# Kernel tuning notes

Measured on AMD Instinct MI355X. Metric: run time of the kernel, lower is better.

## Reference

```python
import jax, jax.numpy as jnp
import numpy as np

B, V, S = 128, 64, 40
D, H, VOC = 256, 256, 20000


def setup_inputs() -> dict:
    key = jax.random.key(0)
    ks = jax.random.split(key, 26)
    g = lambda k, shp: (jax.random.normal(k, shp, dtype=jnp.float32) * 0.02)
    inp = {}
    inp['input_seqs'] = jax.random.randint(ks[0], (B, V, S), 0, VOC + 1)
    inp['mask'] = jnp.zeros((B, V), jnp.float32)
    inp['length'] = jax.random.randint(ks[1], (B,), 1, V + 1)
    inp['seq_time_step'] = jax.random.uniform(ks[2], (B, V), dtype=jnp.float32)
    inp['codemask'] = jnp.zeros((B, V, S), jnp.float32)
    inp['label'] = jax.random.randint(ks[3], (B,), 0, 2)
    # embedding table; padding_idx=-1 in torch == row VOC zeroed
    inp['emb'] = g(ks[4], (VOC + 1, D)).at[VOC].set(0.0)
    # LSTM (single layer, batch_first): torch gate order i,f,g,o
    inp['W_ih'] = g(ks[5], (4 * H, D))
    inp['W_hh'] = g(ks[6], (4 * H, H))
    inp['b_ih'] = g(ks[7], (4 * H,))
    inp['b_hh'] = g(ks[8], (4 * H,))
    # attention projections
    inp['Whk'] = g(ks[9], (D, H))
    inp['bhk'] = g(ks[10], (D,))
    inp['W1'] = g(ks[11], (64, 2 * H))
    inp['b1'] = g(ks[12], (64,))
    inp['W2'] = g(ks[13], (2, 64))
    inp['b2'] = g(ks[14], (2,))
    # classifyer MLP: d -> 4d -> 2d -> 2
    inp['C1W'] = g(ks[15], (4 * D, D))
    inp['C1b'] = g(ks[16], (4 * D,))
    inp['C2W'] = g(ks[17], (2 * D, 4 * D))
    inp['C2b'] = g(ks[18], (2 * D,))
    inp['CoW'] = g(ks[19], (2, 2 * D))
    inp['Cob'] = g(ks[20], (2,))
    return inp


def _lstm(x, W_ih, W_hh, b_ih, b_hh):
    # x: [B,T,D] -> hs: [B,T,H]; torch gate order i,f,g,o
    Bsz = x.shape[0]
    Hd = W_hh.shape[1]
    xg = jnp.einsum('btd,gd->btg', x, W_ih) + b_ih + b_hh  # [B,T,4H]

    def step(carry, xg_t):
        h, c = carry
        gates = xg_t + h @ W_hh.T
        i, f, gg, o = jnp.split(gates, 4, axis=-1)
        i = jax.nn.sigmoid(i); f = jax.nn.sigmoid(f)
        gg = jnp.tanh(gg); o = jax.nn.sigmoid(o)
        c = f * c + i * gg
        h = o * jnp.tanh(c)
        return (h, c), h

    z = jnp.zeros((Bsz, Hd), x.dtype)
    _, hs = jax.lax.scan(step, (z, z), jnp.swapaxes(xg, 0, 1))
    return jnp.swapaxes(hs, 0, 1)


def _classify(h, C1W, C1b, C2W, C2b, CoW, Cob):
    h = jax.nn.relu(h @ C1W.T + C1b)
    h = jax.nn.relu(h @ C2W.T + C2b)
    return h @ CoW.T + Cob


def reference(input_seqs, mask, length, seq_time_step, codemask, label,
              emb, W_ih, W_hh, b_ih, b_hh, Whk, bhk, W1, b1, W2, b2,
              C1W, C1b, C2W, C2b, CoW, Cob):
    # before(): embedding gather -> relu -> sum over codes (eval mode, no dropout)
    v = jax.nn.relu(emb[input_seqs]).sum(-2)  # [B,V,D]
    h = _lstm(v, W_ih, W_hh, b_ih, b_hh)       # [B,V,H]

    # vectorized form of the per-timestep attention loop:
    # bar_v[:,0]=v[:,0]; for i>=1: mix of e_k=v[:,0] and w_hk(h[:,i-1])
    e_k = v[:, :1, :]                                   # [B,1,D]
    wh = h @ Whk.T + bhk                                # [B,V,D]
    wh_prev = wh[:, :-1, :]                             # [B,V-1,D] (h at i-1)
    e_b = jnp.broadcast_to(e_k, wh_prev.shape)
    cat = jnp.concatenate([e_b, wh_prev], axis=-1)      # [B,V-1,2D]
    attn = jax.nn.softmax(jnp.tanh(cat @ W1.T + b1) @ W2.T + b2, axis=-1)
    bar_rest = e_b * attn[..., 0:1] + wh_prev * attn[..., 1:2]
    bar_v = jnp.concatenate([v[:, :1, :], bar_rest], axis=1)  # [B,V,D]

    # GAN stand-in (external injected module): identity
    Dec_V, Gen_V = bar_v, bar_v
    gen_h = _lstm(Gen_V, W_ih, W_hh, b_ih, b_hh)

    og = _classify(h, C1W, C1b, C2W, C2b, CoW, Cob)        # [B,V,2]
    fake = _classify(gen_h, C1W, C1b, C2W, C2b, CoW, Cob)  # [B,V,2]
    final_og = og[:, -1, :]
    final_fake = fake[:, -1, :]
    return (final_og, final_fake, Dec_V, Gen_V, seq_time_step, label)
```

## Files before the change

### kernel.cpp

```cpp
#include <hip/hip_runtime.h>

#define DEV __device__ __forceinline__

typedef float f32x4 __attribute__((ext_vector_type(4)));
typedef short s16x8 __attribute__((ext_vector_type(8)));
typedef short s16x4 __attribute__((ext_vector_type(4)));

DEV unsigned short f2bf(float f){
  unsigned int u = __float_as_uint(f);
  u += 0x7fffu + ((u>>16)&1u);
  return (unsigned short)(u>>16);
}
DEV float bf2f(unsigned short h){ return __uint_as_float(((unsigned int)h)<<16); }

#if __has_builtin(__builtin_amdgcn_rcpf)
DEV float frcp_(float x){ return __builtin_amdgcn_rcpf(x); }
#else
DEV float frcp_(float x){ return 1.f/x; }
#endif
#if __has_builtin(__builtin_amdgcn_exp2f)
DEV float fexp2_(float x){ return __builtin_amdgcn_exp2f(x); }
#else
DEV float fexp2_(float x){ return exp2f(x); }
#endif

DEV float tanh_(float x){
  x = fminf(x, 30.f);
  float e = fexp2_(2.8853900817779268f*x);
  return (e-1.f)*frcp_(e+1.f);
}

DEV unsigned char f2e4m3(float x){
  unsigned int u = __float_as_uint(x);
  unsigned int s = (u>>24)&0x80u;
  unsigned int mag = u & 0x7fffffffu;
  if (mag > 0x43E00000u) mag = 0x43E00000u;
  mag += 0x000FFFFFu + ((mag>>20)&1u);
  int e = (int)(mag>>23) - 120;
  unsigned int m = (mag>>20)&7u;
  unsigned int r = (e<=0) ? 0u : (((unsigned)e<<3)|m);
  return (unsigned char)(s|r);
}

DEV f32x4 mfma_bf16(s16x8 a, s16x8 b, f32x4 c){
  return __builtin_amdgcn_mfma_f32_16x16x32_bf16(a,b,c,0,0,0);
}
DEV f32x4 mfma_fp8(long a, long b, f32x4 c){
  return __builtin_amdgcn_mfma_f32_16x16x32_fp8_fp8(a,b,c,0,0,0);
}

DEV void lds_barrier(){
  asm volatile("s_waitcnt lgkmcnt(0)\n\ts_barrier" ::: "memory");
}

DEV unsigned aload_rlx(unsigned* p){
  return __hip_atomic_load(p, __ATOMIC_RELAXED, __HIP_MEMORY_SCOPE_AGENT);
}
DEV void astore_rel(unsigned* p, unsigned v){
  __hip_atomic_store(p, v, __ATOMIC_RELEASE, __HIP_MEMORY_SCOPE_AGENT);
}
DEV void aadd_rel(unsigned* p, unsigned v){
  __hip_atomic_fetch_add(p, v, __ATOMIC_RELEASE, __HIP_MEMORY_SCOPE_AGENT);
}
DEV void acq_fence(){ __builtin_amdgcn_fence(__ATOMIC_ACQUIRE, "agent"); }
DEV void spin_rlx(unsigned* p, unsigned tgt){
  while (aload_rlx(p) < tgt) __builtin_amdgcn_s_sleep(8);
  asm volatile("" ::: "memory");
}
template<int FENCE>
DEV void block_wait_ge(unsigned* p, unsigned tgt){
  if (threadIdx.x == 0){
    spin_rlx(p, tgt);
    if (FENCE) acq_fence();
  }
  __syncthreads();
}
DEV s16x4 aload64(const unsigned short* p){
  unsigned long long v = __hip_atomic_load((unsigned long long*)(void*)p,
      __ATOMIC_RELAXED, __HIP_MEMORY_SCOPE_AGENT);
  union { unsigned long long u; s16x4 s; } c; c.u = v; return c.s;
}

#define Bx 128
#define Vx 64
#define Sx 40
#define Dx 256
#define Hx 256
#define NVOC 20001

#define OFF_OG   0
#define OFF_FAKE 256
#define OFF_DECV 512
#define OFF_GENV 2097664
#define OFF_STS  4194816
#define OFF_LBL  4203008

#define PW_IH  0
#define PW_HH  262144
#define PW_HK  524288
#define PW_1   589824
#define PC_1   622592
#define PC_2   884736
#define PC_O   1409024
#define P_TOT  1410048

#define HPB 264
#define WHP 272

#define FCT(t) ((t)*32)
#define FBV(t) (2048 + (t)*32)
#define FXG(t) (4096 + (t)*32)
#define FUC    6144
#define FTOT   8192

__global__ void k_cvt_emb(const float* __restrict__ emb, unsigned short* __restrict__ emb16){
  size_t i = (size_t)blockIdx.x*256 + threadIdx.x;
  emb16[i] = f2bf(emb[i]);
}

__global__ void k_pre(const int* __restrict__ seqs, const unsigned short* __restrict__ emb16,
                      unsigned short* __restrict__ v16,
                      float* __restrict__ decv, float* __restrict__ genv,
                      unsigned short* __restrict__ barv16,
                      const float* __restrict__ W_ih, const float* __restrict__ Whh,
                      const float* __restrict__ Whk, const float* __restrict__ W1,
                      const float* __restrict__ C1W, const float* __restrict__ C2W,
                      const float* __restrict__ CoW,
                      unsigned short* __restrict__ pool, unsigned char* __restrict__ whh8,
                      const float* __restrict__ sts, const int* __restrict__ label,
                      float* __restrict__ out, unsigned* __restrict__ flags){
  int bx = blockIdx.x, tid = threadIdx.x;
  if (bx < 8192){
    int bt = bx, d = tid;
    const int* sp = seqs + (size_t)bt*Sx;
    float acc = 0.f;
    #pragma unroll 8
    for (int s=0;s<Sx;s++) acc += fmaxf(bf2f(emb16[(size_t)sp[s]*Dx + d]), 0.f);
    size_t o = (size_t)bt*Dx + d;
    v16[o] = f2bf(acc);
    if ((bt & 63) == 0){ decv[o] = acc; genv[o] = acc; barv16[o] = f2bf(acc); }
    return;
  }
  if (bx < 14724){
    int i = (bx-8192)*256 + tid;
    if (i < P_TOT){
      float v;
      if      (i < PW_HH) v = W_ih[i - PW_IH];
      else if (i < PW_HK) v = Whh [i - PW_HH];
      else if (i < PW_1 ) v = Whk [i - PW_HK];
      else if (i < PC_1 ) v = W1  [i - PW_1 ];
      else if (i < PC_2 ) v = C1W [i - PC_1 ];
      else if (i < PC_O ) v = C2W [i - PC_2 ];
      else                v = CoW [i - PC_O ];
      pool[i] = f2bf(v);
    } else if (i < P_TOT + 262144){
      whh8[i - P_TOT] = f2e4m3(16.f*Whh[i - P_TOT]);
    }
    return;
  }
  for (int i=tid;i<FTOT;i+=256) flags[i] = (i==FBV(0)) ? 1u : 0u;
  for (int i=tid;i<Bx*Vx;i+=256) out[OFF_STS + i] = sts[i];
  if (tid < Bx) out[OFF_LBL + tid] = (float)label[tid];
}

template<int MODE_A, int MODE_C, int RELU>
__global__ void k_gemm(const unsigned short* __restrict__ A, const unsigned short* __restrict__ Bw,
                       const float* __restrict__ bias1, const float* __restrict__ bias2,
                       unsigned short* __restrict__ C, int K, int Ntot, float scale){
  int tid = threadIdx.x, w = tid>>6, l = tid&63, lm = l&15, q = l>>4;
  int m0 = blockIdx.x*64;
  int n0 = blockIdx.y*256 + w*64;
  f32x4 acc[4][4];
  #pragma unroll
  for (int nt=0;nt<4;nt++){
    int n = n0 + nt*16 + lm;
    float bz = bias1 ? bias1[n] : 0.f;
    if (bias2) bz += bias2[n];
    #pragma unroll
    for (int mt=0;mt<4;mt++) acc[mt][nt] = (f32x4){bz,bz,bz,bz};
  }
  const s16x8* Arow[4];
  #pragma unroll
  for (int mt=0;mt<4;mt++){
    int m = m0 + mt*16 + lm;
    size_t off = (MODE_A==0) ? (size_t)m*K : ((size_t)(m&127)*Vx + (m>>7))*(size_t)K;
    Arow[mt] = (const s16x8*)(A + off);
  }
  int kkn = K/32;
  for (int kk=0; kk<kkn; kk++){
    s16x8 bfr[4];
    #pragma unroll
    for (int nt=0;nt<4;nt++){
      int n = n0 + nt*16 + lm;
      bfr[nt] = *(const s16x8*)(Bw + (size_t)n*K + kk*32 + q*8);
    }
    #pragma unroll
    for (int mt=0;mt<4;mt++){
      s16x8 afr = Arow[mt][kk*4 + q];
      #pragma unroll
      for (int nt=0;nt<4;nt++)
        acc[mt][nt] = mfma_bf16(afr, bfr[nt], acc[mt][nt]);
    }
  }
  #pragma unroll
  for (int mt=0;mt<4;mt++){
    int mbase = m0 + mt*16 + q*4;
    #pragma unroll
    for (int nt=0;nt<4;nt++){
      int n = n0 + nt*16 + lm;
      if (MODE_C==0){
        #pragma unroll
        for (int r=0;r<4;r++){
          float val = scale*acc[mt][nt][r];
          if (RELU) val = fmaxf(val, 0.f);
          C[(size_t)(mbase+r)*Ntot + n] = f2bf(val);
        }
      } else {
        int tt = mbase>>7, bb = mbase&127;
        int gg = bb>>4;
        s16x4 sv;
        #pragma unroll
        for (int r=0;r<4;r++) sv[r] = (short)f2bf(scale*acc[mt][nt][r]);
        *(s16x4*)(C + (((size_t)tt*8 + gg)*1024 + n)*16 + (bb&15)) = sv;
      }
    }
  }
}

template<int IS1>
DEV void scan_body(unsigned char* hl, const unsigned char* __restrict__ W8,
                   const unsigned short* __restrict__ xg, unsigned short* __restrict__ hist,
                   int g, unsigned* __restrict__ flags){
  int tid = threadIdx.x;
  int w = tid>>6, l = tid&63, lm = l&15, q = l>>4;
  int j = w*16 + lm;
  for (int i=tid;i<2*16*HPB;i+=1024) hl[i] = 0;
  long Bf[4][8];
  #pragma unroll
  for (int qq=0;qq<4;qq++){
    int n = qq*256 + j;
    #pragma unroll
    for (int kk=0;kk<8;kk++)
      Bf[qq][kk] = *(const long*)(W8 + (size_t)n*256 + kk*32 + q*8);
  }
  float cst[4] = {0.f,0.f,0.f,0.f};
  const unsigned short* xgb = xg + (size_t)g*16384 + q*4;
  s16x4 xc[4], xn[4];
  if (!IS1) block_wait_ge<0>(&flags[FXG(0)], 1);
  #pragma unroll
  for (int qq=0;qq<4;qq++){
    const unsigned short* p = xgb + (qq*256+j)*16;
    xc[qq] = IS1 ? *(const s16x4*)p : aload64(p);
  }
  __syncthreads();
  const float K1 = 1.4426950408889634f/256.f;
  const unsigned char* hrd = hl + lm*HPB + q*8;
  #pragma unroll 1
  for (int t=0;t<Vx;t++){
    if (t < Vx-1){
      if (!IS1) block_wait_ge<0>(&flags[FXG(t+1)], 1);
      #pragma unroll
      for (int qq=0;qq<4;qq++){
        const unsigned short* p = xgb + (size_t)(t+1)*131072 + (qq*256+j)*16;
        xn[qq] = IS1 ? *(const s16x4*)p : aload64(p);
      }
    }
    const unsigned char* hb = hrd + (t&1)*(16*HPB);
    f32x4 a0, a1, a2, a3;
    #pragma unroll
    for (int r=0;r<4;r++){
      a0[r] = bf2f((unsigned short)xc[0][r]);
      a1[r] = bf2f((unsigned short)xc[1][r]);
      a2[r] = bf2f((unsigned short)xc[2][r]);
      a3[r] = bf2f((unsigned short)xc[3][r]);
    }
    #pragma unroll
    for (int kk=0;kk<8;kk++){
      long af = *(const long*)(hb + kk*32);
      a0 = mfma_fp8(af, Bf[0][kk], a0);
      a1 = mfma_fp8(af, Bf[1][kk], a1);
      a2 = mfma_fp8(af, Bf[2][kk], a2);
      a3 = mfma_fp8(af, Bf[3][kk], a3);
    }
    unsigned char* hn = hl + ((t+1)&1)*(16*HPB) + j;
    float hv16[4];
    #pragma unroll
    for (int r=0;r<4;r++){
      float iv = frcp_(1.f + fexp2_(-K1*a0[r]));
      float fv = frcp_(1.f + fexp2_(-K1*a1[r]));
      float eg = fexp2_(2.f*K1*a2[r]);
      float gv = (eg-1.f)*frcp_(eg+1.f);
      float ov = frcp_(1.f + fexp2_(-K1*a3[r]));
      float cv = fv*cst[r] + iv*gv;
      cst[r] = cv;
      float ec = fexp2_(2.8853900817779268f*fminf(cv,30.f));
      float hv = ov*(ec-1.f)*frcp_(ec+1.f);
      hv16[r] = 16.f*hv;
      if (IS1)
        hist[((size_t)t*Bx + g*16 + q*4 + r)*Hx + j] = f2bf(hv);
      else if (t==Vx-1)
        hist[((size_t)(g*16 + q*4 + r))*Hx + j] = f2bf(hv);
    }
#if __has_builtin(__builtin_amdgcn_cvt_pk_fp8_f32)
    int p01 = __builtin_amdgcn_cvt_pk_fp8_f32(hv16[0], hv16[1], 0, false);
    int p23 = __builtin_amdgcn_cvt_pk_fp8_f32(hv16[2], hv16[3], 0, false);
    hn[(q*4+0)*HPB] = (unsigned char)p01;
    hn[(q*4+1)*HPB] = (unsigned char)(p01>>8);
    hn[(q*4+2)*HPB] = (unsigned char)p23;
    hn[(q*4+3)*HPB] = (unsigned char)(p23>>8);
#else
    #pragma unroll
    for (int r=0;r<4;r++) hn[(q*4+r)*HPB] = f2e4m3(hv16[r]);
#endif
    #pragma unroll
    for (int qq=0;qq<4;qq++) xc[qq] = xn[qq];
    if (IS1){
      __syncthreads();
      if (tid == 0) aadd_rel(&flags[FCT(t)], 1);
    } else {
      lds_barrier();
    }
  }
}

DEV void worker_body(unsigned short* whs, int t,
    const unsigned short* __restrict__ hist1, const unsigned short* __restrict__ v16,
    const float* __restrict__ u, const unsigned short* __restrict__ pool,
    const float* __restrict__ bhk, const float* __restrict__ W2, const float* __restrict__ b2,
    const float* __restrict__ b_ih, const float* __restrict__ b_hh,
    float* __restrict__ decv, float* __restrict__ genv,
    unsigned short* __restrict__ barv16, unsigned short* __restrict__ xg2,
    unsigned* flags){
  int tid = threadIdx.x, w = tid>>6, l = tid&63, lm = l&15, q = l>>4;
  if (t < 63){
    block_wait_ge<1>(&flags[FCT(t)], 8);
    int r0 = (w&7)*16, n0 = (w>>3)*128;
    const s16x8* Arow = (const s16x8*)(hist1 + ((size_t)t*Bx + r0 + lm)*Hx);
    f32x4 acc[8];
    #pragma unroll
    for (int nt=0;nt<8;nt++){
      float bz = bhk[n0 + nt*16 + lm];
      acc[nt] = (f32x4){bz,bz,bz,bz};
    }
    #pragma unroll
    for (int kk=0;kk<8;kk++){
      s16x8 afr = Arow[kk*4 + q];
      #pragma unroll
      for (int nt=0;nt<8;nt++){
        int n = n0 + nt*16 + lm;
        s16x8 bfr = *(const s16x8*)(pool + PW_HK + (size_t)n*256 + kk*32 + q*8);
        acc[nt] = mfma_bf16(afr, bfr, acc[nt]);
      }
    }
    #pragma unroll
    for (int nt=0;nt<8;nt++){
      int n = n0 + nt*16 + lm, mb = r0 + q*4;
      #pragma unroll
      for (int r=0;r<4;r++) whs[(size_t)(mb+r)*WHP + n] = f2bf(acc[nt][r]);
    }
    if (tid == 0){ spin_rlx(&flags[FUC], 8); acq_fence(); }
    __syncthreads();
    if (w < 8){
      int m0l = w*16;
      f32x4 a2[4];
      #pragma unroll
      for (int nt=0;nt<4;nt++){
        int n = nt*16 + lm;
        #pragma unroll
        for (int r=0;r<4;r++) a2[nt][r] = u[(size_t)(m0l + q*4 + r)*64 + n];
      }
      #pragma unroll
      for (int kk=0;kk<8;kk++){
        s16x8 afr = *(const s16x8*)(whs + (size_t)(m0l+lm)*WHP + kk*32 + q*8);
        #pragma unroll
        for (int nt=0;nt<4;nt++){
          int n = nt*16 + lm;
          s16x8 bfr = *(const s16x8*)(pool + PW_1 + (size_t)n*512 + 256 + kk*32 + q*8);
          a2[nt] = mfma_bf16(afr, bfr, a2[nt]);
        }
      }
      float p0a[4] = {0,0,0,0}, p1a[4] = {0,0,0,0};
      #pragma unroll
      for (int nt=0;nt<4;nt++){
        int n = nt*16 + lm;
        float w2a = W2[n], w2b = W2[64+n];
        #pragma unroll
        for (int r=0;r<4;r++){
          float z = tanh_(a2[nt][r]);
          p0a[r] += z*w2a; p1a[r] += z*w2b;
        }
      }
      #pragma unroll
      for (int s=1;s<16;s<<=1){
        #pragma unroll
        for (int r=0;r<4;r++){ p0a[r] += __shfl_xor(p0a[r], s, 16); p1a[r] += __shfl_xor(p1a[r], s, 16); }
      }
      float bb0 = b2[0], bb1 = b2[1];
      int d0 = lm*16;
      #pragma unroll
      for (int r=0;r<4;r++){
        int b = m0l + q*4 + r;
        float g0 = p0a[r]+bb0, g1 = p1a[r]+bb1;
        float al0 = frcp_(1.f + fexp2_(1.4426950408889634f*(g1-g0)));
        float al1 = 1.f - al0;
        const unsigned short* ek  = v16 + (size_t)b*Vx*Dx + d0;
        const unsigned short* whp = whs + (size_t)b*WHP + d0;
        size_t ob = ((size_t)b*Vx + (t+1))*Dx + d0;
        #pragma unroll
        for (int c=0;c<2;c++){
          s16x8 e8 = *(const s16x8*)(ek + c*8);
          s16x8 w8 = *(const s16x8*)(whp + c*8);
          s16x8 o16;
          #pragma unroll
          for (int jj=0;jj<8;jj++){
            float o = al0*bf2f((unsigned short)e8[jj]) + al1*bf2f((unsigned short)w8[jj]);
            decv[ob + c*8 + jj] = o;
            genv[ob + c*8 + jj] = o;
            o16[jj] = (short)f2bf(o);
          }
          *(s16x8*)(barv16 + ob + c*8) = o16;
        }
      }
    }
    __syncthreads();
    if (tid == 0) astore_rel(&flags[FBV(t+1)], 1);
  }
  block_wait_ge<1>(&flags[FBV(t)], 1);
  int mh = (w&1)*64, nb = (w>>1)*128;
  const s16x8* Arow2[4];
  #pragma unroll
  for (int mt=0;mt<4;mt++)
    Arow2[mt] = (const s16x8*)(barv16 + ((size_t)(mh + mt*16 + lm)*Vx + t)*Dx);
  #pragma unroll 1
  for (int sc=0; sc<4; sc++){
    int n0 = nb + sc*32;
    f32x4 acc[4][2];
    #pragma unroll
    for (int nt=0;nt<2;nt++){
      int n = n0 + nt*16 + lm;
      float bz = b_ih[n] + b_hh[n];
      #pragma unroll
      for (int mt=0;mt<4;mt++) acc[mt][nt] = (f32x4){bz,bz,bz,bz};
    }
    #pragma unroll
    for (int kk=0;kk<8;kk++){
      s16x8 bfr[2];
      #pragma unroll
      for (int nt=0;nt<2;nt++){
        int n = n0 + nt*16 + lm;
        bfr[nt] = *(const s16x8*)(pool + PW_IH + (size_t)n*256 + kk*32 + q*8);
      }
      #pragma unroll
      for (int mt=0;mt<4;mt++){
        s16x8 afr = Arow2[mt][kk*4 + q];
        acc[mt][0] = mfma_bf16(afr, bfr[0], acc[mt][0]);
        acc[mt][1] = mfma_bf16(afr, bfr[1], acc[mt][1]);
      }
    }
    #pragma unroll
    for (int mt=0;mt<4;mt++){
      int m = mh + mt*16 + q*4;
      int gg = m>>4;
      #pragma unroll
      for (int nt=0;nt<2;nt++){
        int n = n0 + nt*16 + lm;
        s16x4 sv;
        #pragma unroll
        for (int r=0;r<4;r++) sv[r] = (short)f2bf(256.f*acc[mt][nt][r]);
        *(s16x4*)(xg2 + (((size_t)t*8 + gg)*1024 + n)*16 + (m&15)) = sv;
      }
    }
  }
  __syncthreads();
  if (tid == 0) astore_rel(&flags[FXG(t)], 1);
}

__global__ __launch_bounds__(1024) void k_mega(
    const unsigned char* __restrict__ W8,
    const unsigned short* __restrict__ xg1, unsigned short* __restrict__ xg2,
    unsigned short* __restrict__ hist1, unsigned short* __restrict__ h2,
    const unsigned short* __restrict__ v16, float* __restrict__ u,
    const unsigned short* __restrict__ pool,
    const float* __restrict__ bhk, const float* __restrict__ W2, const float* __restrict__ b2,
    const float* __restrict__ b1, const float* __restrict__ b_ih, const float* __restrict__ b_hh,
    float* __restrict__ decv, float* __restrict__ genv, unsigned short* __restrict__ barv16,
    unsigned* __restrict__ flags){
  __shared__ __align__(16) unsigned char smem[69632];
  int blk = blockIdx.x;
  if (blk < 8){
    scan_body<1>(smem, W8, xg1, hist1, blk, flags);
  } else if (blk < 16){
    scan_body<0>(smem, W8, xg2, h2, blk-8, flags);
  } else if (blk < 80){
    worker_body((unsigned short*)smem, blk-16, hist1, v16, u, pool, bhk, W2, b2,
                b_ih, b_hh, decv, genv, barv16, xg2, flags);
  } else {
    int t2 = (blk-80)*1024 + threadIdx.x;
    int b = t2>>6, n = t2&63;
    const s16x8* vr = (const s16x8*)(v16 + (size_t)b*Vx*Dx);
    const s16x8* wr = (const s16x8*)(pool + PW_1 + (size_t)n*512);
    float a = b1[n];
    for (int kk=0;kk<32;kk++){
      s16x8 x = vr[kk], ww = wr[kk];
      #pragma unroll
      for (int jj=0;jj<8;jj++) a += bf2f((unsigned short)x[jj])*bf2f((unsigned short)ww[jj]);
    }
    u[t2] = a;
    __syncthreads();
    if (threadIdx.x == 0) aadd_rel(&flags[FUC], 1);
  }
}

__global__ void k_out(const unsigned short* __restrict__ y2, const unsigned short* __restrict__ CoW16,
                      const float* __restrict__ Cob, float* __restrict__ out){
  int tid = blockIdx.x*256 + threadIdx.x;
  int m = tid>>1, n = tid&1;
  const s16x8* yr = (const s16x8*)(y2 + (size_t)m*512);
  const s16x8* wr = (const s16x8*)(CoW16 + (size_t)n*512);
  float a = Cob[n];
  for (int kk=0;kk<64;kk++){
    s16x8 yv = yr[kk], ww = wr[kk];
    #pragma unroll
    for (int jj=0;jj<8;jj++) a += bf2f((unsigned short)yv[jj])*bf2f((unsigned short)ww[jj]);
  }
  int base = (m < 128) ? (OFF_OG + m*2) : (OFF_FAKE + (m-128)*2);
  out[base + n] = a;
}

extern "C" void kernel_launch(void* const* d_in, const int* in_sizes, int n_in,
                              void* d_out, int out_size, void* d_ws, size_t ws_size,
                              hipStream_t stream) {
  const int*   seqs  = (const int*)d_in[0];
  const float* sts   = (const float*)d_in[3];
  const int*   label = (const int*)d_in[5];
  const float* emb   = (const float*)d_in[6];
  const float* W_ih  = (const float*)d_in[7];
  const float* W_hh  = (const float*)d_in[8];
  const float* b_ih  = (const float*)d_in[9];
  const float* b_hh  = (const float*)d_in[10];
  const float* Whk   = (const float*)d_in[11];
  const float* bhk   = (const float*)d_in[12];
  const float* W1    = (const float*)d_in[13];
  const float* b1    = (const float*)d_in[14];
  const float* W2    = (const float*)d_in[15];
  const float* b2    = (const float*)d_in[16];
  const float* C1b   = (const float*)d_in[18];
  const float* C2b   = (const float*)d_in[20];
  const float* Cob   = (const float*)d_in[22];
  float* out = (float*)d_out;

  char* ws = (char*)d_ws;
  unsigned short* v16    = (unsigned short*)(ws + 0);
  unsigned short* xg1    = (unsigned short*)(ws + (4<<20));
  unsigned short* hist1  = (unsigned short*)(ws + (20<<20));
  unsigned short* barv16 = (unsigned short*)(ws + (25<<20));
  unsigned short* xg2    = (unsigned short*)(ws + (29<<20));
  unsigned short* emb16  = xg2;
  float*          u      = (float*)(ws + (45<<20));
  unsigned char*  whh8   = (unsigned char*)(ws + (45<<20) + (64<<10));
  unsigned*       flags  = (unsigned*)(ws + (45<<20) + (384<<10));
  unsigned short* pool   = (unsigned short*)(ws + (46<<20));
  unsigned short* y1     = xg1;
  unsigned short* y2     = xg1 + 262144;

  unsigned short* h2 = hist1 + (size_t)Vx*Bx*Hx;
  unsigned short* X  = hist1 + (size_t)(Vx-1)*Bx*Hx;

  float* decv = out + OFF_DECV;
  float* genv = out + OFF_GENV;

  k_cvt_emb<<<dim3(NVOC), dim3(256), 0, stream>>>(emb, emb16);
  k_pre<<<dim3(14725), dim3(256), 0, stream>>>(seqs, emb16, v16, decv, genv, barv16,
      W_ih, W_hh, Whk, W1, (const float*)d_in[17], (const float*)d_in[19],
      (const float*)d_in[21], pool, whh8, sts, label, out, flags);
  k_gemm<1,1,0><<<dim3(128,4), dim3(256), 0, stream>>>(v16, pool+PW_IH, b_ih, b_hh, xg1, 256, 1024, 256.f);
  k_mega<<<dim3(88), dim3(1024), 0, stream>>>(whh8, xg1, xg2, hist1, h2, v16, u, pool,
      bhk, W2, b2, b1, b_ih, b_hh, decv, genv, barv16, flags);
  k_gemm<0,0,1><<<dim3(4,4), dim3(256), 0, stream>>>(X, pool+PC_1, C1b, nullptr, y1, 256, 1024, 1.f);
  k_gemm<0,0,1><<<dim3(4,2), dim3(256), 0, stream>>>(y1, pool+PC_2, C2b, nullptr, y2, 1024, 512, 1.f);
  k_out<<<dim3(2), dim3(256), 0, stream>>>(y2, pool+PC_O, Cob, out);
}
```

Baseline: 537.4 us.

## Replace release/acquire fences with relaxed agent-scope atomics for cross-block data

Every value passed between blocks (hidden-state history, u, bar_v, xg2) is now written and read with relaxed agent-scope atomic loads and stores. This lets the flag signals drop their release/acquire semantics and the acquire fence, removing cache writeback and invalidate costs on the serial scan critical path. History stores are packed into 32-bit words through a lane shuffle, and 128-bit loads are split into two 64-bit atomic loads. The risk is memory-ordering correctness, because relaxed flags give no formal happens-before guarantee.

```diff
diff --git a/kernel.cpp b/kernel.cpp
--- a/kernel.cpp
+++ b/kernel.cpp
@@ -56,29 +56,44 @@
 DEV unsigned aload_rlx(unsigned* p){
   return __hip_atomic_load(p, __ATOMIC_RELAXED, __HIP_MEMORY_SCOPE_AGENT);
 }
-DEV void astore_rel(unsigned* p, unsigned v){
-  __hip_atomic_store(p, v, __ATOMIC_RELEASE, __HIP_MEMORY_SCOPE_AGENT);
-}
-DEV void aadd_rel(unsigned* p, unsigned v){
-  __hip_atomic_fetch_add(p, v, __ATOMIC_RELEASE, __HIP_MEMORY_SCOPE_AGENT);
-}
-DEV void acq_fence(){ __builtin_amdgcn_fence(__ATOMIC_ACQUIRE, "agent"); }
+DEV void astore_rlx(unsigned* p, unsigned v){
+  __hip_atomic_store(p, v, __ATOMIC_RELAXED, __HIP_MEMORY_SCOPE_AGENT);
+}
+DEV void aadd_rlx(unsigned* p, unsigned v){
+  __hip_atomic_fetch_add(p, v, __ATOMIC_RELAXED, __HIP_MEMORY_SCOPE_AGENT);
+}
 DEV void spin_rlx(unsigned* p, unsigned tgt){
   while (aload_rlx(p) < tgt) __builtin_amdgcn_s_sleep(8);
   asm volatile("" ::: "memory");
 }
-template<int FENCE>
 DEV void block_wait_ge(unsigned* p, unsigned tgt){
-  if (threadIdx.x == 0){
-    spin_rlx(p, tgt);
-    if (FENCE) acq_fence();
-  }
+  if (threadIdx.x == 0) spin_rlx(p, tgt);
   __syncthreads();
 }
-DEV s16x4 aload64(const unsigned short* p){
+DEV void wt_store32(unsigned short* p, unsigned v){
+  __hip_atomic_store((unsigned*)(void*)p, v, __ATOMIC_RELAXED, __HIP_MEMORY_SCOPE_AGENT);
+}
+DEV void wt_store32f(float* p, float v){
+  __hip_atomic_store(p, v, __ATOMIC_RELAXED, __HIP_MEMORY_SCOPE_AGENT);
+}
+DEV float wt_load32f(const float* p){
+  return __hip_atomic_load((float*)p, __ATOMIC_RELAXED, __HIP_MEMORY_SCOPE_AGENT);
+}
+DEV void wt_store64(unsigned short* p, s16x4 v){
+  union { s16x4 s; unsigned long long u; } c; c.s = v;
+  __hip_atomic_store((unsigned long long*)(void*)p, c.u, __ATOMIC_RELAXED, __HIP_MEMORY_SCOPE_AGENT);
+}
+DEV s16x4 wt_load64(const unsigned short* p){
   unsigned long long v = __hip_atomic_load((unsigned long long*)(void*)p,
       __ATOMIC_RELAXED, __HIP_MEMORY_SCOPE_AGENT);
   union { unsigned long long u; s16x4 s; } c; c.u = v; return c.s;
+}
+DEV s16x8 wt_load128(const unsigned short* p){
+  s16x4 lo = wt_load64(p), hi = wt_load64(p+4);
+  s16x8 r;
+  r[0]=lo[0]; r[1]=lo[1]; r[2]=lo[2]; r[3]=lo[3];
+  r[4]=hi[0]; r[5]=hi[1]; r[6]=hi[2]; r[7]=hi[3];
+  return r;
 }
 
 #define Bx 128
@@ -246,11 +261,11 @@
   float cst[4] = {0.f,0.f,0.f,0.f};
   const unsigned short* xgb = xg + (size_t)g*16384 + q*4;
   s16x4 xc[4], xn[4];
-  if (!IS1) block_wait_ge<0>(&flags[FXG(0)], 1);
+  if (!IS1) block_wait_ge(&flags[FXG(0)], 1);
   #pragma unroll
   for (int qq=0;qq<4;qq++){
     const unsigned short* p = xgb + (qq*256+j)*16;
-    xc[qq] = IS1 ? *(const s16x4*)p : aload64(p);
+    xc[qq] = IS1 ? *(const s16x4*)p : wt_load64(p);
   }
   __syncthreads();
   const float K1 = 1.4426950408889634f/256.f;
@@ -258,11 +273,11 @@
   #pragma unroll 1
   for (int t=0;t<Vx;t++){
     if (t < Vx-1){
-      if (!IS1) block_wait_ge<0>(&flags[FXG(t+1)], 1);
+      if (!IS1) block_wait_ge(&flags[FXG(t+1)], 1);
       #pragma unroll
       for (int qq=0;qq<4;qq++){
         const unsigned short* p = xgb + (size_t)(t+1)*131072 + (qq*256+j)*16;
-        xn[qq] = IS1 ? *(const s16x4*)p : aload64(p);
+        xn[qq] = IS1 ? *(const s16x4*)p : wt_load64(p);
       }
     }
     const unsigned char* hb = hrd + (t&1)*(16*HPB);
@@ -296,10 +311,16 @@
       float ec = fexp2_(2.8853900817779268f*fminf(cv,30.f));
       float hv = ov*(ec-1.f)*frcp_(ec+1.f);
       hv16[r] = 16.f*hv;
-      if (IS1)
-        hist[((size_t)t*Bx + g*16 + q*4 + r)*Hx + j] = f2bf(hv);
-      else if (t==Vx-1)
-        hist[((size_t)(g*16 + q*4 + r))*Hx + j] = f2bf(hv);
+      unsigned short h16 = f2bf(hv);
+      if (IS1){
+        unsigned short pr = (unsigned short)__shfl_xor((int)h16, 1, 64);
+        if (!(lm & 1)){
+          unsigned pv = (unsigned)h16 | ((unsigned)pr<<16);
+          wt_store32(&hist[((size_t)t*Bx + g*16 + q*4 + r)*Hx + j], pv);
+        }
+      } else if (t==Vx-1){
+        hist[((size_t)(g*16 + q*4 + r))*Hx + j] = h16;
+      }
     }
 #if __has_builtin(__builtin_amdgcn_cvt_pk_fp8_f32)
     int p01 = __builtin_amdgcn_cvt_pk_fp8_f32(hv16[0], hv16[1], 0, false);
@@ -316,7 +337,7 @@
     for (int qq=0;qq<4;qq++) xc[qq] = xn[qq];
     if (IS1){
       __syncthreads();
-      if (tid == 0) aadd_rel(&flags[FCT(t)], 1);
+      if (tid == 0) aadd_rlx(&flags[FCT(t)], 1);
     } else {
       lds_barrier();
     }
@@ -325,7 +346,7 @@
 
 DEV void worker_body(unsigned short* whs, int t,
     const unsigned short* __restrict__ hist1, const unsigned short* __restrict__ v16,
-    const float* __restrict__ u, const unsigned short* __restrict__ pool,
+    float* __restrict__ u, const unsigned short* __restrict__ pool,
     const float* __restrict__ bhk, const float* __restrict__ W2, const float* __restrict__ b2,
     const float* __restrict__ b_ih, const float* __restrict__ b_hh,
     float* __restrict__ decv, float* __restrict__ genv,
@@ -333,9 +354,9 @@
     unsigned* flags){
   int tid = threadIdx.x, w = tid>>6, l = tid&63, lm = l&15, q = l>>4;
   if (t < 63){
-    block_wait_ge<1>(&flags[FCT(t)], 8);
+    block_wait_ge(&flags[FCT(t)], 8);
     int r0 = (w&7)*16, n0 = (w>>3)*128;
-    const s16x8* Arow = (const s16x8*)(hist1 + ((size_t)t*Bx + r0 + lm)*Hx);
+    const unsigned short* Abase = hist1 + ((size_t)t*Bx + r0 + lm)*Hx;
     f32x4 acc[8];
     #pragma unroll
     for (int nt=0;nt<8;nt++){
@@ -344,7 +365,7 @@
     }
     #pragma unroll
     for (int kk=0;kk<8;kk++){
-      s16x8 afr = Arow[kk*4 + q];
+      s16x8 afr = wt_load128(Abase + (kk*4 + q)*8);
       #pragma unroll
       for (int nt=0;nt<8;nt++){
         int n = n0 + nt*16 + lm;
@@ -358,7 +379,7 @@
       #pragma unroll
       for (int r=0;r<4;r++) whs[(size_t)(mb+r)*WHP + n] = f2bf(acc[nt][r]);
     }
-    if (tid == 0){ spin_rlx(&flags[FUC], 8); acq_fence(); }
+    if (tid == 0) spin_rlx(&flags[FUC], 8);
     __syncthreads();
     if (w < 8){
       int m0l = w*16;
@@ -367,7 +388,7 @@
       for (int nt=0;nt<4;nt++){
         int n = nt*16 + lm;
         #pragma unroll
-        for (int r=0;r<4;r++) a2[nt][r] = u[(size_t)(m0l + q*4 + r)*64 + n];
+        for (int r=0;r<4;r++) a2[nt][r] = wt_load32f(u + (size_t)(m0l + q*4 + r)*64 + n);
       }
       #pragma unroll
       for (int kk=0;kk<8;kk++){
@@ -410,27 +431,28 @@
         for (int c=0;c<2;c++){
           s16x8 e8 = *(const s16x8*)(ek + c*8);
           s16x8 w8 = *(const s16x8*)(whp + c*8);
-          s16x8 o16;
+          s16x4 olo, ohi;
           #pragma unroll
           for (int jj=0;jj<8;jj++){
             float o = al0*bf2f((unsigned short)e8[jj]) + al1*bf2f((unsigned short)w8[jj]);
             decv[ob + c*8 + jj] = o;
             genv[ob + c*8 + jj] = o;
-            o16[jj] = (short)f2bf(o);
+            if (jj<4) olo[jj] = (short)f2bf(o); else ohi[jj-4] = (short)f2bf(o);
           }
-          *(s16x8*)(barv16 + ob + c*8) = o16;
+          wt_store64(barv16 + ob + c*8, olo);
+          wt_store64(barv16 + ob + c*8 + 4, ohi);
         }
       }
     }
     __syncthreads();
-    if (tid == 0) astore_rel(&flags[FBV(t+1)], 1);
-  }
-  block_wait_ge<1>(&flags[FBV(t)], 1);
+    if (tid == 0) astore_rlx(&flags[FBV(t+1)], 1);
+  }
+  block_wait_ge(&flags[FBV(t)], 1);
   int mh = (w&1)*64, nb = (w>>1)*128;
-  const s16x8* Arow2[4];
+  const unsigned short* A2base[4];
   #pragma unroll
   for (int mt=0;mt<4;mt++)
-    Arow2[mt] = (const s16x8*)(barv16 + ((size_t)(mh + mt*16 + lm)*Vx + t)*Dx);
+    A2base[mt] = barv16 + ((size_t)(mh + mt*16 + lm)*Vx + t)*Dx;
   #pragma unroll 1
   for (int sc=0; sc<4; sc++){
     int n0 = nb + sc*32;
@@ -452,7 +474,7 @@
       }
       #pragma unroll
       for (int mt=0;mt<4;mt++){
-        s16x8 afr = Arow2[mt][kk*4 + q];
+        s16x8 afr = wt_load128(A2base[mt] + (kk*4 + q)*8);
         acc[mt][0] = mfma_bf16(afr, bfr[0], acc[mt][0]);
         acc[mt][1] = mfma_bf16(afr, bfr[1], acc[mt][1]);
       }
@@ -467,12 +489,12 @@
         s16x4 sv;
         #pragma unroll
         for (int r=0;r<4;r++) sv[r] = (short)f2bf(256.f*acc[mt][nt][r]);
-        *(s16x4*)(xg2 + (((size_t)t*8 + gg)*1024 + n)*16 + (m&15)) = sv;
+        wt_store64(xg2 + (((size_t)t*8 + gg)*1024 + n)*16 + (m&15), sv);
       }
     }
   }
   __syncthreads();
-  if (tid == 0) astore_rel(&flags[FXG(t)], 1);
+  if (tid == 0) astore_rlx(&flags[FXG(t)], 1);
 }
 
 __global__ __launch_bounds__(1024) void k_mega(
@@ -505,9 +527,9 @@
       #pragma unroll
       for (int jj=0;jj<8;jj++) a += bf2f((unsigned short)x[jj])*bf2f((unsigned short)ww[jj]);
     }
-    u[t2] = a;
+    wt_store32f(u + t2, a);
     __syncthreads();
-    if (threadIdx.x == 0) aadd_rel(&flags[FUC], 1);
+    if (threadIdx.x == 0) aadd_rlx(&flags[FUC], 1);
   }
 }
 
```

Measured after the change: 603.3 us. 12.3% more time.
